# Performance work log

Hardware: AMD Instinct MI355X
Metric: run time of the kernel (lower is better)

The kernel has to match this reference:

```python
import jax, jax.numpy as jnp
import numpy as np

EPS = 1e-5

def _ln(x, g, b):
    mu = jnp.mean(x, axis=-1, keepdims=True)
    var = jnp.mean(jnp.square(x - mu), axis=-1, keepdims=True)
    return (x - mu) * jax.lax.rsqrt(var + EPS) * g + b

def _mha(xq, xkv, Wq, bq, Wk, bk, Wv, bv, Wo, bo, causal):
    # Wq/Wk/Wv: [H,E,D]; per-head linear projections (no 1/sqrt(d) scaling, faithful to source)
    q = jnp.einsum('bse,hed->bhsd', xq, Wq) + bq[None, :, None, :]
    k = jnp.einsum('bte,hed->bhtd', xkv, Wk) + bk[None, :, None, :]
    v = jnp.einsum('bte,hed->bhtd', xkv, Wv) + bv[None, :, None, :]
    s = jnp.einsum('bhsd,bhtd->bhst', q, k)
    if causal:
        S, T = s.shape[-2], s.shape[-1]
        keep = jnp.tril(jnp.ones((S, T), dtype=bool))  # intended causal mask (source had inverted-mask bug -> NaNs)
        s = jnp.where(keep[None, None], s, jnp.finfo(s.dtype).min)
    w = jax.nn.softmax(s, axis=-1)
    o = jnp.einsum('bhst,bhtd->bhsd', w, v)
    B, H, S, D = o.shape
    o = o.transpose(0, 2, 1, 3).reshape(B, S, H * D)  # concat heads in order, matches torch.cat
    return o @ Wo + bo

def setup_inputs() -> dict:
    B, S, T, E, H, D, F = 4, 1024, 1024, 1024, 16, 64, 4096
    key = jax.random.key(0)
    ks = iter(jax.random.split(key, 40))
    def w(shape, scale=0.02):
        return (scale * jax.random.normal(next(ks), shape)).astype(jnp.float32)
    inp = {
        'x': w((B, S, E), 1.0),
        'enc': w((B, T, E), 1.0),
        'ln1_g': jnp.ones((E,), jnp.float32), 'ln1_b': jnp.zeros((E,), jnp.float32),
        'ln2_g': jnp.ones((E,), jnp.float32), 'ln2_b': jnp.zeros((E,), jnp.float32),
        'ln3_g': jnp.ones((E,), jnp.float32), 'ln3_b': jnp.zeros((E,), jnp.float32),
        'Wq1': w((H, E, D)), 'bq1': jnp.zeros((H, D), jnp.float32),
        'Wk1': w((H, E, D)), 'bk1': jnp.zeros((H, D), jnp.float32),
        'Wv1': w((H, E, D)), 'bv1': jnp.zeros((H, D), jnp.float32),
        'Wo1': w((E, E)), 'bo1': jnp.zeros((E,), jnp.float32),
        'Wq2': w((H, E, D)), 'bq2': jnp.zeros((H, D), jnp.float32),
        'Wk2': w((H, E, D)), 'bk2': jnp.zeros((H, D), jnp.float32),
        'Wv2': w((H, E, D)), 'bv2': jnp.zeros((H, D), jnp.float32),
        'Wo2': w((E, E)), 'bo2': jnp.zeros((E,), jnp.float32),
        'Wup': w((E, F)), 'bup': jnp.zeros((F,), jnp.float32),
        'Wdown': w((F, E)), 'bdown': jnp.zeros((E,), jnp.float32),
    }
    return inp

def reference(x, enc, ln1_g, ln1_b, ln2_g, ln2_b, ln3_g, ln3_b,
              Wq1, bq1, Wk1, bk1, Wv1, bv1, Wo1, bo1,
              Wq2, bq2, Wk2, bk2, Wv2, bv2, Wo2, bo2,
              Wup, bup, Wdown, bdown):
    h = _ln(x, ln1_g, ln1_b)
    x = x + _mha(h, h, Wq1, bq1, Wk1, bk1, Wv1, bv1, Wo1, bo1, causal=True)
    h = _ln(x, ln2_g, ln2_b)
    x = x + _mha(h, enc, Wq2, bq2, Wk2, bk2, Wv2, bv2, Wo2, bo2, causal=False)
    h = _ln(x, ln3_g, ln3_b)
    ff = jax.nn.gelu(h @ Wup + bup, approximate=False) @ Wdown + bdown  # dropout is identity in eval
    return x + ff
```

## Files before the change

kernel.cpp:

```cpp
#include <hip/hip_runtime.h>
#include <math.h>

typedef unsigned short u16;
typedef __bf16  bf16x8 __attribute__((ext_vector_type(8)));
typedef float   f32x4  __attribute__((ext_vector_type(4)));

__device__ __forceinline__ u16 f2bf(float f) {
  unsigned u = __float_as_uint(f);
  u += 0x7fffu + ((u >> 16) & 1u);
  return (u16)(u >> 16);
}
__device__ __forceinline__ void gl_lds16(const void* g, void* l) {
  __builtin_amdgcn_global_load_lds((__attribute__((address_space(1))) void*)(void*)g,
                                   (__attribute__((address_space(3))) void*)l, 16u, 0, 0u);
}
__device__ __forceinline__ f32x4 mfma16(bf16x8 a, bf16x8 b, f32x4 c) {
  return __builtin_amdgcn_mfma_f32_16x16x32_bf16(a, b, c, 0, 0, 0);
}

__global__ __launch_bounds__(256) void ln_kernel(const float* __restrict__ x,
    const float* __restrict__ g, const float* __restrict__ b, u16* __restrict__ out) {
  const long row = blockIdx.x;
  const int t = threadIdx.x;
  const float4 v = ((const float4*)(x + row * 1024))[t];
  float s  = v.x + v.y + v.z + v.w;
  float sq = v.x*v.x + v.y*v.y + v.z*v.z + v.w*v.w;
#pragma unroll
  for (int m = 1; m < 64; m <<= 1) { s += __shfl_xor(s, m); sq += __shfl_xor(sq, m); }
  __shared__ float ss[4], ssq[4];
  const int wave = t >> 6;
  if ((t & 63) == 0) { ss[wave] = s; ssq[wave] = sq; }
  __syncthreads();
  s  = ss[0] + ss[1] + ss[2] + ss[3];
  sq = ssq[0] + ssq[1] + ssq[2] + ssq[3];
  const float mu = s * (1.0f / 1024.0f);
  const float rs = rsqrtf(sq * (1.0f / 1024.0f) - mu * mu + 1e-5f);
  const float4 gg = ((const float4*)g)[t];
  const float4 bb = ((const float4*)b)[t];
  ushort4 o;
  o.x = f2bf((v.x - mu) * rs * gg.x + bb.x);
  o.y = f2bf((v.y - mu) * rs * gg.y + bb.y);
  o.z = f2bf((v.z - mu) * rs * gg.z + bb.z);
  o.w = f2bf((v.w - mu) * rs * gg.w + bb.w);
  ((ushort4*)(out + row * 1024))[t] = o;
}

__global__ __launch_bounds__(256) void cast_kernel(const float* __restrict__ in, u16* __restrict__ out) {
  const long i = ((long)blockIdx.x * 256 + threadIdx.x) * 4;
  const float4 v = *(const float4*)(in + i);
  ushort4 o;
  o.x = f2bf(v.x); o.y = f2bf(v.y); o.z = f2bf(v.z); o.w = f2bf(v.w);
  *(ushort4*)(out + i) = o;
}

__global__ __launch_bounds__(256) void tp_kernel(const float* __restrict__ in,
    u16* __restrict__ out, int C, long in_bs, long out_bs, int out_ld) {
  __shared__ u16 tile[64][65];
  in  += (long)blockIdx.z * in_bs;
  out += (long)blockIdx.z * out_bs;
  const int r0 = blockIdx.y << 6, c0 = blockIdx.x << 6;
  const int t = threadIdx.x;
  const int lr = t >> 4, lc = (t & 15) << 2;
#pragma unroll
  for (int i = 0; i < 4; i++) {
    const int row = lr + i * 16;
    const float4 v = *(const float4*)(in + (long)(r0 + row) * C + c0 + lc);
    tile[row][lc + 0] = f2bf(v.x); tile[row][lc + 1] = f2bf(v.y);
    tile[row][lc + 2] = f2bf(v.z); tile[row][lc + 3] = f2bf(v.w);
  }
  __syncthreads();
#pragma unroll
  for (int i = 0; i < 4; i++) {
    const int cc = lr + i * 16;
    ushort4 o;
    o.x = tile[lc + 0][cc]; o.y = tile[lc + 1][cc];
    o.z = tile[lc + 2][cc]; o.w = tile[lc + 3][cc];
    *(ushort4*)(out + (long)(c0 + cc) * out_ld + r0 + lc) = o;
  }
}

__global__ __launch_bounds__(256) void tp3_kernel(const float* __restrict__ p0,
    const float* __restrict__ p1, const float* __restrict__ p2, u16* __restrict__ out) {
  __shared__ u16 tile[64][65];
  const int z = blockIdx.z;
  const float* in = (z < 16 ? p0 : z < 32 ? p1 : p2) + (long)(z & 15) * 65536;
  u16* o = out + (long)z * 65536;
  const int r0 = blockIdx.y << 6;
  const int t = threadIdx.x;
  const int lr = t >> 4, lc = (t & 15) << 2;
#pragma unroll
  for (int i = 0; i < 4; i++) {
    const int row = lr + i * 16;
    const float4 v = *(const float4*)(in + (long)(r0 + row) * 64 + lc);
    tile[row][lc + 0] = f2bf(v.x); tile[row][lc + 1] = f2bf(v.y);
    tile[row][lc + 2] = f2bf(v.z); tile[row][lc + 3] = f2bf(v.w);
  }
  __syncthreads();
#pragma unroll
  for (int i = 0; i < 4; i++) {
    const int cc = lr + i * 16;
    ushort4 ov;
    ov.x = tile[lc + 0][cc]; ov.y = tile[lc + 1][cc];
    ov.z = tile[lc + 2][cc]; ov.w = tile[lc + 3][cc];
    *(ushort4*)(o + (long)cc * 1024 + r0 + lc) = ov;
  }
}

template<int MFRAG, int MODE>
__global__ __launch_bounds__(256, 2) void gemm_kernel(
    const u16* __restrict__ A, const u16* __restrict__ BT,
    const float* __restrict__ b0, const float* __restrict__ b1, const float* __restrict__ b2,
    const float* __restrict__ res,
    u16* __restrict__ o0, u16* __restrict__ o1, u16* __restrict__ o2,
    float* __restrict__ of, int M, int N, int K)
{
  constexpr int BM = MFRAG * 32;
  __shared__ __bf16 As[BM * 64];
  __shared__ __bf16 Bs[128 * 64];
  const int tid = threadIdx.x;
  const int wave = tid >> 6, lane = tid & 63;
  const int g = lane >> 4, li = lane & 15;

  const int gx = gridDim.x;
  const int nwg = gx * gridDim.y;
  const int lin = blockIdx.y * gx + blockIdx.x;
  const int cpx = nwg >> 3;
  const int swz = (lin & 7) * cpx + (lin >> 3);
  const int bxs = swz % gx, bys = swz / gx;

  const long m0 = (long)bys * BM;
  const int  n0 = bxs << 7;
  const int  wr = wave >> 1, wc = wave & 1;

  f32x4 acc[MFRAG][4] = {};

  const u16* Ag = A + (m0 + wave * (MFRAG * 8) + (lane >> 3)) * K + ((lane & 7) << 3);
  const u16* Bg = BT + ((long)(n0 + wave * 32 + (lane >> 3))) * K + ((lane & 7) << 3);
  __bf16* AsW = As + wave * (MFRAG * 512);
  __bf16* BsW = Bs + wave * 2048;

  for (int k0 = 0; k0 < K; k0 += 64) {
#pragma unroll
    for (int i = 0; i < MFRAG; i++)
      gl_lds16(Ag + (long)i * 8 * K + k0, AsW + i * 512);
#pragma unroll
    for (int i = 0; i < 4; i++)
      gl_lds16(Bg + (long)i * 8 * K + k0, BsW + i * 512);
    __syncthreads();
#pragma unroll
    for (int kk = 0; kk < 2; kk++) {
      bf16x8 af[MFRAG], bv[4];
#pragma unroll
      for (int m = 0; m < MFRAG; m++)
        af[m] = *(const bf16x8*)&As[(wr * (MFRAG * 16) + m * 16 + li) * 64 + kk * 32 + g * 8];
#pragma unroll
      for (int n = 0; n < 4; n++)
        bv[n] = *(const bf16x8*)&Bs[(wc * 64 + n * 16 + li) * 64 + kk * 32 + g * 8];
#pragma unroll
      for (int m = 0; m < MFRAG; m++)
#pragma unroll
        for (int n = 0; n < 4; n++)
          acc[m][n] = mfma16(af[m], bv[n], acc[m][n]);
    }
    __syncthreads();
  }

#pragma unroll
  for (int m = 0; m < MFRAG; m++) {
#pragma unroll
    for (int n = 0; n < 4; n++) {
      const int col = n0 + wc * 64 + n * 16 + li;
#pragma unroll
      for (int r = 0; r < 4; r++) {
        const int row = (int)m0 + wr * (MFRAG * 16) + m * 16 + g * 4 + r;
        float v = acc[m][n][r];
        if constexpr (MODE == 0 || MODE == 1) {
          const int sel = col >> 10, cl = col & 1023;
          v += (MODE == 0 ? (sel == 0 ? b0 : sel == 1 ? b1 : b2)
                          : (sel == 0 ? b0 : b1))[cl];
          const int bI = row >> 10, sI = row & 1023, hI = cl >> 6, dI = cl & 63;
          const long bhI = (long)(bI * 16 + hI);
          const int qsel = (MODE == 0) ? 0 : -1;
          if (sel == qsel) {
            o0[(bhI * 1024 + sI) * 64 + dI] = f2bf(v);
          } else if (sel == qsel + 1) {
            u16* Kp = (MODE == 0) ? o1 : o0;
            Kp[(bhI * 1024 + sI) * 64 + (dI ^ ((sI & 7) << 3))] = f2bf(v);
          } else {
            u16* Vp = (MODE == 0) ? o2 : o1;
            Vp[(bhI * 64 + dI) * 1024 + (sI & ~63) + ((sI & 63) ^ ((dI & 7) << 3))] = f2bf(v);
          }
        } else if constexpr (MODE == 2) {
          v += b0[col];
          const int bI = row >> 10, sI = row & 1023, hI = col >> 6, dI = col & 63;
          o0[((long)(bI * 16 + hI) * 1024 + sI) * 64 + dI] = f2bf(v);
        } else if constexpr (MODE == 3) {
          v += b0[col];
          const long idx = (long)row * N + col;
          of[idx] = v + res[idx];
        } else {
          v += b0[col];
          const float gl = 0.5f * v * (1.0f + erff(v * 0.70710678118654752f));
          o0[(long)row * N + col] = f2bf(gl);
        }
      }
    }
  }
}

__global__ __launch_bounds__(256, 2) void attn_kernel(
    const u16* __restrict__ Q, const u16* __restrict__ Kb,
    const u16* __restrict__ VT, u16* __restrict__ O, const int causal)
{
  __shared__ u16 Ks[2][4096];
  __shared__ u16 Vs[2][4096];
  __shared__ u16 Ps[4][1024];
  const int tid = threadIdx.x;
  const int wave = tid >> 6, lane = tid & 63;
  const int g = lane >> 4, li = lane & 15;
  const int qt = blockIdx.x, bh = blockIdx.y;
  const int b_ = bh >> 4, h_ = bh & 15;
  const int q_lo = qt * 64 + wave * 16;

  const u16* Qp = Q + ((long)bh * 1024 + q_lo + li) * 64 + g * 8;
  const bf16x8 aq0 = *(const bf16x8*)Qp;
  const bf16x8 aq1 = *(const bf16x8*)(Qp + 32);

  f32x4 acc[4] = {};
  float mrun[4] = {-1e30f, -1e30f, -1e30f, -1e30f};
  float lrun[4] = {0.f, 0.f, 0.f, 0.f};

  const u16* Kbh = Kb + (long)bh * 65536;
  const u16* Vbh = VT + (long)bh * 65536;
  const int swl = (li & 7) << 3;

  const int nk = causal ? (qt + 1) : 16;

#pragma unroll
  for (int i = 0; i < 2; i++) {
    const int bc = i * 256 + wave * 64;
    gl_lds16(Kbh + (long)(bc + lane) * 8, &Ks[0][bc * 8]);
    const int ci = bc + lane, d = ci >> 3, c = ci & 7;
    gl_lds16(Vbh + (long)d * 1024 + c * 8, &Vs[0][bc * 8]);
  }
  __syncthreads();

  for (int kt = 0; kt < nk; kt++) {
    const int buf = kt & 1;
    const int k0 = kt * 64;
    if (kt + 1 < nk) {
      const int nb = buf ^ 1;
#pragma unroll
      for (int i = 0; i < 2; i++) {
        const int bc = i * 256 + wave * 64;
        gl_lds16(Kbh + (long)(kt + 1) * 4096 + (long)(bc + lane) * 8, &Ks[nb][bc * 8]);
        const int ci = bc + lane, d = ci >> 3, c = ci & 7;
        gl_lds16(Vbh + (long)d * 1024 + (kt + 1) * 64 + c * 8, &Vs[nb][bc * 8]);
      }
    }

    f32x4 s[4] = {};
#pragma unroll
    for (int n = 0; n < 4; n++) {
      const u16* kp = &Ks[buf][(n * 16 + li) * 64];
      const bf16x8 bk0 = *(const bf16x8*)(kp + ((g * 8) ^ swl));
      const bf16x8 bk1 = *(const bf16x8*)(kp + ((32 + g * 8) ^ swl));
      s[n] = mfma16(aq0, bk0, s[n]);
      s[n] = mfma16(aq1, bk1, s[n]);
    }

    if (causal && k0 + 63 > q_lo) {
#pragma unroll
      for (int n = 0; n < 4; n++) {
        const int key = k0 + n * 16 + li;
#pragma unroll
        for (int r = 0; r < 4; r++)
          if (key > q_lo + g * 4 + r) s[n][r] = -1e30f;
      }
    }

    float pmax[4];
#pragma unroll
    for (int r = 0; r < 4; r++) {
      float pm = fmaxf(fmaxf(s[0][r], s[1][r]), fmaxf(s[2][r], s[3][r]));
      pm = fmaxf(pm, __shfl_xor(pm, 1));
      pm = fmaxf(pm, __shfl_xor(pm, 2));
      pm = fmaxf(pm, __shfl_xor(pm, 4));
      pm = fmaxf(pm, __shfl_xor(pm, 8));
      pmax[r] = pm;
    }
    const bool need = (pmax[0] > mrun[0] + 8.f) || (pmax[1] > mrun[1] + 8.f) ||
                      (pmax[2] > mrun[2] + 8.f) || (pmax[3] > mrun[3] + 8.f);
    if (__any(need)) {
#pragma unroll
      for (int r = 0; r < 4; r++) {
        const float mnew = fmaxf(mrun[r], pmax[r]);
        const float sc = __expf(mrun[r] - mnew);
        mrun[r] = mnew;
        lrun[r] *= sc;
        acc[0][r] *= sc; acc[1][r] *= sc; acc[2][r] *= sc; acc[3][r] *= sc;
      }
    }
#pragma unroll
    for (int r = 0; r < 4; r++) {
      const int q = g * 4 + r;
      const int swq = (q & 7) << 3;
      const float p0 = __expf(s[0][r] - mrun[r]);
      const float p1 = __expf(s[1][r] - mrun[r]);
      const float p2 = __expf(s[2][r] - mrun[r]);
      const float p3 = __expf(s[3][r] - mrun[r]);
      u16* pw = &Ps[wave][q * 64];
      pw[(li)      ^ swq] = f2bf(p0);
      pw[(16 + li) ^ swq] = f2bf(p1);
      pw[(32 + li) ^ swq] = f2bf(p2);
      pw[(48 + li) ^ swq] = f2bf(p3);
      float rs_ = (p0 + p1) + (p2 + p3);
      rs_ += __shfl_xor(rs_, 1);
      rs_ += __shfl_xor(rs_, 2);
      rs_ += __shfl_xor(rs_, 4);
      rs_ += __shfl_xor(rs_, 8);
      lrun[r] += rs_;
    }

    const bf16x8 pa0 = *(const bf16x8*)&Ps[wave][li * 64 + ((g * 8) ^ swl)];
    const bf16x8 pa1 = *(const bf16x8*)&Ps[wave][li * 64 + ((32 + g * 8) ^ swl)];
#pragma unroll
    for (int n = 0; n < 4; n++) {
      const u16* vp = &Vs[buf][(n * 16 + li) * 64];
      const bf16x8 v0 = *(const bf16x8*)(vp + ((g * 8) ^ swl));
      const bf16x8 v1 = *(const bf16x8*)(vp + ((32 + g * 8) ^ swl));
      acc[n] = mfma16(pa0, v0, acc[n]);
      acc[n] = mfma16(pa1, v1, acc[n]);
    }
    __syncthreads();
  }

#pragma unroll
  for (int r = 0; r < 4; r++) {
    const int q = q_lo + g * 4 + r;
    const float inv = 1.0f / lrun[r];
#pragma unroll
    for (int n = 0; n < 4; n++)
      O[((long)b_ * 1024 + q) * 1024 + h_ * 64 + n * 16 + li] = f2bf(acc[n][r] * inv);
  }
}

extern "C" void kernel_launch(void* const* d_in, const int* in_sizes, int n_in,
                              void* d_out, int out_size, void* d_ws, size_t ws_size,
                              hipStream_t stream) {
  const float* x     = (const float*)d_in[0];
  const float* enc   = (const float*)d_in[1];
  const float* ln1_g = (const float*)d_in[2];
  const float* ln1_b = (const float*)d_in[3];
  const float* ln2_g = (const float*)d_in[4];
  const float* ln2_b = (const float*)d_in[5];
  const float* ln3_g = (const float*)d_in[6];
  const float* ln3_b = (const float*)d_in[7];
  const float* Wq1 = (const float*)d_in[8];  const float* bq1 = (const float*)d_in[9];
  const float* Wk1 = (const float*)d_in[10]; const float* bk1 = (const float*)d_in[11];
  const float* Wv1 = (const float*)d_in[12]; const float* bv1 = (const float*)d_in[13];
  const float* Wo1 = (const float*)d_in[14]; const float* bo1 = (const float*)d_in[15];
  const float* Wq2 = (const float*)d_in[16]; const float* bq2 = (const float*)d_in[17];
  const float* Wk2 = (const float*)d_in[18]; const float* bk2 = (const float*)d_in[19];
  const float* Wv2 = (const float*)d_in[20]; const float* bv2 = (const float*)d_in[21];
  const float* Wo2 = (const float*)d_in[22]; const float* bo2 = (const float*)d_in[23];
  const float* Wup = (const float*)d_in[24]; const float* bup = (const float*)d_in[25];
  const float* Wdn = (const float*)d_in[26]; const float* bdn = (const float*)d_in[27];

  char* ws = (char*)d_ws;
  const size_t MB = 1ull << 20;
  u16*   wpack  = (u16*)(ws);
  u16*   enc_bf = (u16*)(ws + 8 * MB);
  u16*   h_bf   = (u16*)(ws + 16 * MB);
  u16*   Qb     = (u16*)(ws + 24 * MB);
  u16*   Kbf    = (u16*)(ws + 32 * MB);
  u16*   VTb    = (u16*)(ws + 40 * MB);
  u16*   att_o  = (u16*)(ws + 48 * MB);
  float* x2     = (float*)(ws + 56 * MB);
  float* x3     = (float*)(ws + 72 * MB);
  u16*   ffmid  = (u16*)(ws + 24 * MB);
  u16*   wo_t   = wpack + 3 * 1024 * 1024;

  const dim3 T(256);

  ln_kernel<<<4096, T, 0, stream>>>(x, ln1_g, ln1_b, h_bf);
  cast_kernel<<<4096, T, 0, stream>>>(enc, enc_bf);
  tp3_kernel<<<dim3(1, 16, 48), T, 0, stream>>>(Wq1, Wk1, Wv1, wpack);
  gemm_kernel<4, 0><<<dim3(24, 32), T, 0, stream>>>(h_bf, wpack, bq1, bk1, bv1, nullptr,
      Qb, Kbf, VTb, nullptr, 4096, 3072, 1024);
  attn_kernel<<<dim3(16, 64), T, 0, stream>>>(Qb, Kbf, VTb, att_o, 1);
  tp_kernel<<<dim3(16, 16, 1), T, 0, stream>>>(Wo1, wo_t, 1024, 0L, 0L, 1024);
  gemm_kernel<2, 3><<<dim3(8, 64), T, 0, stream>>>(att_o, wo_t, bo1, nullptr, nullptr, x,
      nullptr, nullptr, nullptr, x2, 4096, 1024, 1024);

  ln_kernel<<<4096, T, 0, stream>>>(x2, ln2_g, ln2_b, h_bf);
  tp3_kernel<<<dim3(1, 16, 48), T, 0, stream>>>(Wq2, Wk2, Wv2, wpack);
  gemm_kernel<2, 2><<<dim3(8, 64), T, 0, stream>>>(h_bf, wpack, bq2, nullptr, nullptr, nullptr,
      Qb, nullptr, nullptr, nullptr, 4096, 1024, 1024);
  gemm_kernel<4, 1><<<dim3(16, 32), T, 0, stream>>>(enc_bf, wpack + 1024 * 1024, bk2, bv2, nullptr, nullptr,
      Kbf, VTb, nullptr, nullptr, 4096, 2048, 1024);
  attn_kernel<<<dim3(16, 64), T, 0, stream>>>(Qb, Kbf, VTb, att_o, 0);
  tp_kernel<<<dim3(16, 16, 1), T, 0, stream>>>(Wo2, wo_t, 1024, 0L, 0L, 1024);
  gemm_kernel<2, 3><<<dim3(8, 64), T, 0, stream>>>(att_o, wo_t, bo2, nullptr, nullptr, x2,
      nullptr, nullptr, nullptr, x3, 4096, 1024, 1024);

  ln_kernel<<<4096, T, 0, stream>>>(x3, ln3_g, ln3_b, h_bf);
  tp_kernel<<<dim3(64, 16, 1), T, 0, stream>>>(Wup, wpack, 4096, 0L, 0L, 1024);
  gemm_kernel<4, 4><<<dim3(32, 32), T, 0, stream>>>(h_bf, wpack, bup, nullptr, nullptr, nullptr,
      ffmid, nullptr, nullptr, nullptr, 4096, 4096, 1024);
  tp_kernel<<<dim3(16, 64, 1), T, 0, stream>>>(Wdn, wpack, 1024, 0L, 0L, 4096);
  gemm_kernel<4, 3><<<dim3(8, 32), T, 0, stream>>>(ffmid, wpack, bdn, nullptr, nullptr, x3,
      nullptr, nullptr, nullptr, (float*)d_out, 4096, 1024, 4096);
}
```

Before: 651.0 us.

## Double-buffer GEMM LDS tiles and drop workgroup swizzle

Splits the GEMM shared-memory tiles into two buffers so the global-to-LDS load for the next K-slice is issued before computing on the current one, overlapping memory traffic with MFMA work. It also removes the block-index swizzle that grouped workgroups for L2 locality and uses plain blockIdx mapping. This doubles LDS use per block, which may limit the two-blocks-per-CU occupancy. Loss of the swizzle may also hurt cache reuse. The loop assumes K is a multiple of 128.

```diff
diff --git a/kernel.cpp b/kernel.cpp
--- a/kernel.cpp
+++ b/kernel.cpp
@@ -115,53 +115,56 @@
     float* __restrict__ of, int M, int N, int K)
 {
   constexpr int BM = MFRAG * 32;
-  __shared__ __bf16 As[BM * 64];
-  __shared__ __bf16 Bs[128 * 64];
+  __shared__ __bf16 As[2][BM * 64];
+  __shared__ __bf16 Bs[2][128 * 64];
   const int tid = threadIdx.x;
   const int wave = tid >> 6, lane = tid & 63;
   const int g = lane >> 4, li = lane & 15;
-
-  const int gx = gridDim.x;
-  const int nwg = gx * gridDim.y;
-  const int lin = blockIdx.y * gx + blockIdx.x;
-  const int cpx = nwg >> 3;
-  const int swz = (lin & 7) * cpx + (lin >> 3);
-  const int bxs = swz % gx, bys = swz / gx;
-
-  const long m0 = (long)bys * BM;
-  const int  n0 = bxs << 7;
+  const long m0 = (long)blockIdx.y * BM;
+  const int  n0 = blockIdx.x << 7;
   const int  wr = wave >> 1, wc = wave & 1;
 
   f32x4 acc[MFRAG][4] = {};
 
   const u16* Ag = A + (m0 + wave * (MFRAG * 8) + (lane >> 3)) * K + ((lane & 7) << 3);
   const u16* Bg = BT + ((long)(n0 + wave * 32 + (lane >> 3))) * K + ((lane & 7) << 3);
-  __bf16* AsW = As + wave * (MFRAG * 512);
-  __bf16* BsW = Bs + wave * 2048;
-
-  for (int k0 = 0; k0 < K; k0 += 64) {
+  const int aw = wave * (MFRAG * 512);
+  const int bw = wave * 2048;
+
+  auto stage = [&](int buf, int kk0) {
 #pragma unroll
     for (int i = 0; i < MFRAG; i++)
-      gl_lds16(Ag + (long)i * 8 * K + k0, AsW + i * 512);
+      gl_lds16(Ag + (long)i * 8 * K + kk0, &As[buf][aw + i * 512]);
 #pragma unroll
     for (int i = 0; i < 4; i++)
-      gl_lds16(Bg + (long)i * 8 * K + k0, BsW + i * 512);
-    __syncthreads();
+      gl_lds16(Bg + (long)i * 8 * K + kk0, &Bs[buf][bw + i * 512]);
+  };
+  auto compute = [&](int buf) {
 #pragma unroll
     for (int kk = 0; kk < 2; kk++) {
       bf16x8 af[MFRAG], bv[4];
 #pragma unroll
       for (int m = 0; m < MFRAG; m++)
-        af[m] = *(const bf16x8*)&As[(wr * (MFRAG * 16) + m * 16 + li) * 64 + kk * 32 + g * 8];
+        af[m] = *(const bf16x8*)&As[buf][(wr * (MFRAG * 16) + m * 16 + li) * 64 + kk * 32 + g * 8];
 #pragma unroll
       for (int n = 0; n < 4; n++)
-        bv[n] = *(const bf16x8*)&Bs[(wc * 64 + n * 16 + li) * 64 + kk * 32 + g * 8];
+        bv[n] = *(const bf16x8*)&Bs[buf][(wc * 64 + n * 16 + li) * 64 + kk * 32 + g * 8];
 #pragma unroll
       for (int m = 0; m < MFRAG; m++)
 #pragma unroll
         for (int n = 0; n < 4; n++)
           acc[m][n] = mfma16(af[m], bv[n], acc[m][n]);
     }
+  };
+
+  stage(0, 0);
+  __syncthreads();
+  for (int k0 = 0; k0 < K; k0 += 128) {
+    stage(1, k0 + 64);
+    compute(0);
+    __syncthreads();
+    if (k0 + 128 < K) stage(0, k0 + 128);
+    compute(1);
     __syncthreads();
   }
 
```

New measurement: 660.8 us. Within noise of the previous version (+1.5%).
